# Performance work log

Hardware: AMD Instinct MI355X
Metric: run time of the kernel (lower is better)

Reference implementation:

```python
import jax, jax.numpy as jnp
import numpy as np

P = 3; Q = 3                 # spline degrees (deg_p, deg_q)
OUT_U = 64; OUT_V = 64       # surface evaluation grid
W_CTRL = 1.0; W_SURF = 1.0
B = 1024; MU_MAX = 32; MV_MAX = 32
EPS = 1e-5                   # SurfEval samples u,v in [eps, 1-eps]


def _open_uniform_knots(n_valid, degree, n_max):
    """Clamped open-uniform knot vector for n_valid ctrl pts, padded to static
    length n_max+degree+1. Entries beyond the valid span are clamped to 1.0,
    which makes the padded basis functions identically zero on [eps, 1-eps]."""
    L = n_valid + degree + 1  # true (ragged) knot count, traced int
    k = jnp.arange(n_max + degree + 1)
    interior = k.astype(jnp.float32) / (L - 1).astype(jnp.float32)
    return jnp.where(k <= degree, 0.0, jnp.where(k >= L - 1 - degree, 1.0, interior))


def _bspline_basis(kv, degree, u):
    """Cox-de Boor, vectorized over u. kv: (n_max+degree+1,), u: (U,).
    Returns (U, n_max) basis matrix; padded columns are exactly zero."""
    N = ((u[None, :] >= kv[:-1, None]) & (u[None, :] < kv[1:, None])).astype(jnp.float32)
    for d in range(1, degree + 1):
        m = N.shape[0] - 1  # number of basis funcs at this level
        den1 = kv[d:d + m] - kv[:m]
        den2 = kv[d + 1:d + 1 + m] - kv[1:1 + m]
        s1 = jnp.where((den1 > 0)[:, None],
                       (u[None, :] - kv[:m, None]) / jnp.where(den1 > 0, den1, 1.0)[:, None], 0.0)
        s2 = jnp.where((den2 > 0)[:, None],
                       (kv[d + 1:d + 1 + m, None] - u[None, :]) / jnp.where(den2 > 0, den2, 1.0)[:, None], 0.0)
        N = s1 * N[:m] + s2 * N[1:m + 1]
    return N.T  # (U, n_max)


def _eval_surface(ctrl, mask_b, u, v):
    """NURBS surface eval for one sample with ragged (Mu_i, Mv_i) via padded
    knots/basis; unit weights => rational division by basis partition sum."""
    mu = jnp.maximum(jnp.sum(jnp.any(mask_b > 0, axis=1)), P + 1)
    mv = jnp.maximum(jnp.sum(jnp.any(mask_b > 0, axis=0)), Q + 1)
    Bu = _bspline_basis(_open_uniform_knots(mu, P, MU_MAX), P, u)  # (OUT_U, MU_MAX)
    Bv = _bspline_basis(_open_uniform_knots(mv, Q, MV_MAX), Q, v)  # (OUT_V, MV_MAX)
    num = jnp.einsum('ui,vj,ijd->uvd', Bu, Bv, ctrl)               # (OUT_U, OUT_V, 3)
    den = Bu.sum(-1)[:, None] * Bv.sum(-1)[None, :]                # unit-weight denom
    return num / den[..., None]


def setup_inputs() -> dict:
    key = jax.random.key(0)
    k1, k2, k3, k4, k5 = jax.random.split(key, 5)
    # ragged true control sizes per sample, >= degree+1
    mu = jax.random.randint(k1, (B,), P + 1, MU_MAX + 1)
    mv = jax.random.randint(k2, (B,), Q + 1, MV_MAX + 1)
    mask = ((jnp.arange(MU_MAX)[None, :, None] < mu[:, None, None]) &
            (jnp.arange(MV_MAX)[None, None, :] < mv[:, None, None])).astype(jnp.float32)
    ctrl_pred_pad = jax.random.normal(k3, (B, MU_MAX, MV_MAX, 3), jnp.float32)
    ctrl_gt_pad = jax.random.normal(k4, (B, MU_MAX, MV_MAX, 3), jnp.float32)
    xyz_samples = jax.random.normal(k5, (B, OUT_U, OUT_V, 3), jnp.float32)
    return {"ctrl_pred_pad": ctrl_pred_pad, "ctrl_gt_pad": ctrl_gt_pad,
            "mask": mask, "xyz_samples": xyz_samples}


def reference(ctrl_pred_pad, ctrl_gt_pad, mask, xyz_samples):
    # masked control-point MSE
    diff2 = ((ctrl_pred_pad - ctrl_gt_pad) ** 2).sum(-1)
    loss_ctrl = (diff2 * mask).sum() / jnp.maximum(mask.sum() * 3.0, 1.0)
    # batched ragged surface evaluation
    u = jnp.linspace(EPS, 1.0 - EPS, OUT_U)
    v = jnp.linspace(EPS, 1.0 - EPS, OUT_V)
    surf = jax.vmap(lambda c, m: _eval_surface(c, m, u, v))(ctrl_pred_pad, mask)
    loss_surf = jnp.mean((surf.reshape(B, -1, 3) - xyz_samples.reshape(B, -1, 3)) ** 2)
    total = W_CTRL * loss_ctrl + W_SURF * loss_surf  # original computes total BEFORE nan-guard
    bad = jnp.isnan(surf).any() | jnp.isinf(surf).any()
    surf_mse = jnp.where(bad, jnp.float32(1e6), loss_surf)
    return total, loss_ctrl, surf_mse
```

## Files before the change

### kernel.cpp

```cpp
#include <hip/hip_runtime.h>
#include <math.h>

#define MU_MAXC 32
#define MV_MAXC 32
#define OUT_UC  64
#define OUT_VC  64
#define DEG     3
#define NKNOT   (MU_MAXC + DEG + 1)
#define EPSV    1e-5f

__global__ void zero_ws_kernel(double* acc, int* bad) {
    acc[0] = 0.0; acc[1] = 0.0; acc[2] = 0.0; bad[0] = 0;
}

__device__ __forceinline__ float kv_at(int k, int L) {
    return (k <= DEG) ? 0.f : ((k >= L - 1 - DEG) ? 1.f : (float)k / (float)(L - 1));
}

template <int MODE>
__launch_bounds__(256)
__global__ void nurbs_loss_kernel(const float* __restrict__ ctrl_pred,
                                  const float* __restrict__ ctrl_gt,
                                  const float* __restrict__ mask,
                                  const float* __restrict__ xyz,
                                  double* __restrict__ pd, int G,
                                  int* __restrict__ badp)
{
    const int bb  = blockIdx.x;
    const int s   = bb >> 1;
    const int h   = bb & 1;
    const int tid = threadIdx.x;

    __shared__ float s_tmp[32 * MV_MAXC * 3];
    __shared__ float s_Bu4[4 * 32];
    __shared__ float s_Bv4[4 * OUT_VC];
    __shared__ int   s_uoff[32];
    __shared__ int   s_voff[OUT_VC];
    __shared__ float s_invSumBu[32];
    __shared__ int   s_rowany[MU_MAXC];
    __shared__ int   s_colany[MV_MAXC];
    __shared__ int   s_mu, s_mv, s_bad;
    __shared__ float s_wred[4], s_wred2[4];
    __shared__ float s_ctrl_diff, s_ctrl_mask;

    if (tid < 32) { s_rowany[tid] = 0; s_colany[tid] = 0; }
    if (tid == 0) s_bad = 0;
    __syncthreads();

    float lsum_mask, lsum_diff = 0.f;
    float4 mm;
    {
        mm = ((const float4*)(mask + (size_t)s * 1024))[tid];
        lsum_mask = mm.x + mm.y + mm.z + mm.w;
        const int row = tid >> 3;
        const int colb = (tid & 7) * 4;
        if (lsum_mask > 0.f) s_rowany[row] = 1;
        if (mm.x > 0.f) s_colany[colb + 0] = 1;
        if (mm.y > 0.f) s_colany[colb + 1] = 1;
        if (mm.z > 0.f) s_colany[colb + 2] = 1;
        if (mm.w > 0.f) s_colany[colb + 3] = 1;
    }
    if ((tid >> 7) == h) {
        const float4* p4 = (const float4*)(ctrl_pred + (size_t)s * 3072);
        const float4* g4 = (const float4*)(ctrl_gt   + (size_t)s * 3072);
        const float4 pa = p4[3 * tid + 0], pb = p4[3 * tid + 1], pc = p4[3 * tid + 2];
        const float4 ga = g4[3 * tid + 0], gb = g4[3 * tid + 1], gc = g4[3 * tid + 2];
        const float a0 = pa.x - ga.x, a1 = pa.y - ga.y, a2 = pa.z - ga.z;
        const float b0 = pa.w - ga.w, b1 = pb.x - gb.x, b2 = pb.y - gb.y;
        const float c0 = pb.z - gb.z, c1 = pb.w - gb.w, c2 = pc.x - gc.x;
        const float e0 = pc.y - gc.y, e1 = pc.z - gc.z, e2 = pc.w - gc.w;
        lsum_diff = mm.x * (a0 * a0 + a1 * a1 + a2 * a2)
                  + mm.y * (b0 * b0 + b1 * b1 + b2 * b2)
                  + mm.z * (c0 * c0 + c1 * c1 + c2 * c2)
                  + mm.w * (e0 * e0 + e1 * e1 + e2 * e2);
    }
    lsum_mask *= 0.5f;
    #pragma unroll
    for (int off = 32; off > 0; off >>= 1) {
        lsum_mask += __shfl_down(lsum_mask, off);
        lsum_diff += __shfl_down(lsum_diff, off);
    }
    if ((tid & 63) == 0) { s_wred[tid >> 6] = lsum_mask; s_wred2[tid >> 6] = lsum_diff; }
    __syncthreads();

    if (tid == 0) {
        int cu = 0, cv = 0;
        #pragma unroll
        for (int i = 0; i < 32; i++) { cu += s_rowany[i]; cv += s_colany[i]; }
        s_mu = cu > (DEG + 1) ? cu : (DEG + 1);
        s_mv = cv > (DEG + 1) ? cv : (DEG + 1);
        s_ctrl_mask = s_wred[0] + s_wred[1] + s_wred[2] + s_wred[3];
        s_ctrl_diff = s_wred2[0] + s_wred2[1] + s_wred2[2] + s_wred2[3];
    }
    __syncthreads();

    if (tid < 96) {
        const bool isV = tid < 64;
        const int t = isV ? tid : (tid - 64);
        const int gidx = isV ? t : (32 * h + t);
        const int L = (isV ? s_mv : s_mu) + DEG + 1;
        const float step = (1.f - 2.f * EPSV) / 63.f;
        const float uu = (gidx == 63) ? (1.f - EPSV) : (EPSV + step * (float)gidx);

        int span = DEG;
        #pragma unroll
        for (int k = DEG + 1; k < NKNOT - 1; k++)
            if (kv_at(k, L) <= uu) span = k;

        float left[DEG + 1], right[DEG + 1];
        #pragma unroll
        for (int j = 1; j <= DEG; j++) {
            left[j]  = uu - kv_at(span + 1 - j, L);
            right[j] = kv_at(span + j, L) - uu;
        }
        float N4[DEG + 1];
        N4[0] = 1.f;
        #pragma unroll
        for (int j = 1; j <= DEG; j++) {
            float saved = 0.f;
            #pragma unroll
            for (int r = 0; r < j; r++) {
                const float temp = N4[r] / (right[r + 1] + left[j - r]);
                N4[r] = saved + right[r + 1] * temp;
                saved = left[j - r] * temp;
            }
            N4[j] = saved;
        }
        const float sum = N4[0] + N4[1] + N4[2] + N4[3];
        const float invs = 1.0f / sum;
        const int off = span - DEG;
        if (isV) {
            #pragma unroll
            for (int r = 0; r < 4; r++) s_Bv4[r * 64 + t] = N4[r] * invs;
            s_voff[t] = off;
        } else {
            #pragma unroll
            for (int r = 0; r < 4; r++) s_Bu4[r * 32 + t] = N4[r];
            s_uoff[t] = off; s_invSumBu[t] = invs;
        }
    }
    __syncthreads();

    {
        const float4* ctrl4 = (const float4*)(ctrl_pred + (size_t)s * 3072);
        float4* tmp4 = (float4*)s_tmp;
        #pragma unroll
        for (int k = 0; k < 3; k++) {
            const int flat4 = tid + 256 * k;
            const int lu = flat4 / 24;
            const int q = flat4 - lu * 24;
            const int off = s_uoff[lu];
            const float w0 = s_Bu4[0 * 32 + lu];
            const float w1 = s_Bu4[1 * 32 + lu];
            const float w2 = s_Bu4[2 * 32 + lu];
            const float w3 = s_Bu4[3 * 32 + lu];
            const float4 c0 = ctrl4[(off + 0) * 24 + q];
            const float4 c1 = ctrl4[(off + 1) * 24 + q];
            const float4 c2 = ctrl4[(off + 2) * 24 + q];
            const float4 c3 = ctrl4[(off + 3) * 24 + q];
            float4 a;
            a.x = w0 * c0.x + w1 * c1.x + w2 * c2.x + w3 * c3.x;
            a.y = w0 * c0.y + w1 * c1.y + w2 * c2.y + w3 * c3.y;
            a.z = w0 * c0.z + w1 * c1.z + w2 * c2.z + w3 * c3.z;
            a.w = w0 * c0.w + w1 * c1.w + w2 * c2.w + w3 * c3.w;
            tmp4[flat4] = a;
        }
    }
    __syncthreads();

    float lsum_surf = 0.f;
    int bad = 0;
    {
        const int vg   = (tid & 15) * 4;
        const int lug0 = tid >> 4;
        float w[4][4]; int vo[4];
        #pragma unroll
        for (int c = 0; c < 4; c++) {
            vo[c] = s_voff[vg + c] * 3;
            #pragma unroll
            for (int r = 0; r < 4; r++) w[c][r] = s_Bv4[r * 64 + vg + c];
        }
        #pragma unroll
        for (int k = 0; k < 2; k++) {
            const int lu = lug0 + 16 * k;
            const int u  = 32 * h + lu;
            const float inv = s_invSumBu[lu];
            const float* tp = &s_tmp[lu * 96];
            const float4* x4 = (const float4*)(xyz + ((size_t)s * 4096 + u * 64 + vg) * 3);
            const float4 xa = x4[0], xb = x4[1], xc = x4[2];
            float px[4], py[4], pz[4];
            px[0] = xa.x; py[0] = xa.y; pz[0] = xa.z;
            px[1] = xa.w; py[1] = xb.x; pz[1] = xb.y;
            px[2] = xb.z; py[2] = xb.w; pz[2] = xc.x;
            px[3] = xc.y; py[3] = xc.z; pz[3] = xc.w;
            #pragma unroll
            for (int c = 0; c < 4; c++) {
                const float* tpc = tp + vo[c];
                const float n0 = w[c][0] * tpc[0] + w[c][1] * tpc[3] + w[c][2] * tpc[6] + w[c][3] * tpc[9];
                const float n1 = w[c][0] * tpc[1] + w[c][1] * tpc[4] + w[c][2] * tpc[7] + w[c][3] * tpc[10];
                const float n2 = w[c][0] * tpc[2] + w[c][1] * tpc[5] + w[c][2] * tpc[8] + w[c][3] * tpc[11];
                const float x0 = n0 * inv, x1 = n1 * inv, x2 = n2 * inv;
                const float d0 = x0 - px[c];
                const float d1 = x1 - py[c];
                const float d2 = x2 - pz[c];
                lsum_surf += d0 * d0 + d1 * d1 + d2 * d2;
                if (!isfinite(x0) || !isfinite(x1) || !isfinite(x2)) bad = 1;
            }
        }
    }
    #pragma unroll
    for (int off = 32; off > 0; off >>= 1)
        lsum_surf += __shfl_down(lsum_surf, off);
    if ((tid & 63) == 0) s_wred[tid >> 6] = lsum_surf;
    if (bad) atomicOr(&s_bad, 1);
    __syncthreads();

    if (tid == 0) {
        const double surf = (double)s_wred[0] + s_wred[1] + s_wred[2] + s_wred[3];
        if (MODE == 0) {
            pd[bb]          = (double)s_ctrl_diff;
            pd[G + bb]      = (double)s_ctrl_mask;
            pd[2 * G + bb]  = surf;
            badp[bb]        = s_bad;
        } else {
            atomicAdd(&pd[0], (double)s_ctrl_diff);
            atomicAdd(&pd[1], (double)s_ctrl_mask);
            atomicAdd(&pd[2], surf);
            if (s_bad) atomicOr(badp, 1);
        }
    }
}

__global__ void finalize_partials_kernel(const double* __restrict__ pd,
                                         const int* __restrict__ badp,
                                         float* __restrict__ out, int G, int Bcnt)
{
    __shared__ double sd0[4], sd1[4], sd2[4];
    __shared__ int sb[4];
    const int tid = threadIdx.x;
    double a0 = 0.0, a1 = 0.0, a2 = 0.0; int bad = 0;
    for (int i = tid; i < G; i += 256) {
        a0 += pd[i]; a1 += pd[G + i]; a2 += pd[2 * G + i];
        bad |= badp[i];
    }
    #pragma unroll
    for (int off = 32; off > 0; off >>= 1) {
        a0 += __shfl_down(a0, off);
        a1 += __shfl_down(a1, off);
        a2 += __shfl_down(a2, off);
        bad |= __shfl_down(bad, off);
    }
    if ((tid & 63) == 0) { const int w = tid >> 6; sd0[w] = a0; sd1[w] = a1; sd2[w] = a2; sb[w] = bad; }
    __syncthreads();
    if (tid == 0) {
        double d0 = 0, d1 = 0, d2 = 0; int bb = 0;
        #pragma unroll
        for (int i = 0; i < 4; i++) { d0 += sd0[i]; d1 += sd1[i]; d2 += sd2[i]; bb |= sb[i]; }
        const double denc = d1 * 3.0;
        const double lc = d0 / (denc > 1.0 ? denc : 1.0);
        const double ls = d2 / ((double)Bcnt * OUT_UC * OUT_VC * 3.0);
        out[0] = (float)(lc + ls);
        out[1] = (float)lc;
        out[2] = bb ? 1.0e6f : (float)ls;
    }
}

__global__ void finalize_atomic_kernel(const double* __restrict__ acc,
                                       const int* __restrict__ bad,
                                       float* __restrict__ out, int Bcnt)
{
    const double denc = acc[1] * 3.0;
    const double lc = acc[0] / (denc > 1.0 ? denc : 1.0);
    const double ls = acc[2] / ((double)Bcnt * OUT_UC * OUT_VC * 3.0);
    out[0] = (float)(lc + ls);
    out[1] = (float)lc;
    out[2] = bad[0] ? 1.0e6f : (float)ls;
}

extern "C" void kernel_launch(void* const* d_in, const int* in_sizes, int n_in,
                              void* d_out, int out_size, void* d_ws, size_t ws_size,
                              hipStream_t stream)
{
    const float* pred = (const float*)d_in[0];
    const float* gt   = (const float*)d_in[1];
    const float* mask = (const float*)d_in[2];
    const float* xyz  = (const float*)d_in[3];
    const int Bcnt = in_sizes[2] / (MU_MAXC * MV_MAXC);
    const int G = 2 * Bcnt;

    double* pd = (double*)d_ws;
    float* out = (float*)d_out;

    const size_t need = (size_t)3 * G * sizeof(double) + (size_t)G * sizeof(int);
    if (ws_size >= need) {
        int* badp = (int*)(pd + 3 * G);
        hipLaunchKernelGGL((nurbs_loss_kernel<0>), dim3(G), dim3(256), 0, stream,
                           pred, gt, mask, xyz, pd, G, badp);
        hipLaunchKernelGGL(finalize_partials_kernel, dim3(1), dim3(256), 0, stream,
                           pd, badp, out, G, Bcnt);
    } else {
        int* badp = (int*)(pd + 3);
        hipLaunchKernelGGL(zero_ws_kernel, dim3(1), dim3(1), 0, stream, pd, badp);
        hipLaunchKernelGGL((nurbs_loss_kernel<1>), dim3(G), dim3(256), 0, stream,
                           pred, gt, mask, xyz, pd, G, badp);
        hipLaunchKernelGGL(finalize_atomic_kernel, dim3(1), dim3(1), 0, stream,
                           pd, badp, out, Bcnt);
    }
}
```

Before: 115.2 us.

## Prefetch xyz samples into LDS via async global_load_lds at kernel start

The kernel now issues the xyz sample tile for its half-surface at the very beginning as direct global-to-LDS loads. It also hoists the ctrl_pred/ctrl_gt loads ahead of the first barrier, so the memory latency overlaps the mask reduction and basis computation instead of being exposed in the final loss loop. This costs an extra 24KB of LDS per block, which may reduce occupancy. Correctness relies on the async LDS writes being complete at the first __syncthreads.

```diff
diff --git a/kernel.cpp b/kernel.cpp
--- a/kernel.cpp
+++ b/kernel.cpp
@@ -31,7 +31,8 @@
     const int h   = bb & 1;
     const int tid = threadIdx.x;
 
-    __shared__ float s_tmp[32 * MV_MAXC * 3];
+    __shared__ __align__(16) float s_xyz[32 * OUT_VC * 3];
+    __shared__ __align__(16) float s_tmp[32 * MV_MAXC * 3];
     __shared__ float s_Bu4[4 * 32];
     __shared__ float s_Bv4[4 * OUT_VC];
     __shared__ int   s_uoff[32];
@@ -45,13 +46,33 @@
 
     if (tid < 32) { s_rowany[tid] = 0; s_colany[tid] = 0; }
     if (tid == 0) s_bad = 0;
-    __syncthreads();
-
-    float lsum_mask, lsum_diff = 0.f;
-    float4 mm;
+
+    const float4 mm = ((const float4*)(mask + (size_t)s * 1024))[tid];
+    float4 pa, pb, pc, ga, gb, gc;
+    const int mine = ((tid >> 7) == h);
+    if (mine) {
+        const float4* p4 = (const float4*)(ctrl_pred + (size_t)s * 3072);
+        const float4* g4 = (const float4*)(ctrl_gt   + (size_t)s * 3072);
+        pa = p4[3 * tid + 0]; pb = p4[3 * tid + 1]; pc = p4[3 * tid + 2];
+        ga = g4[3 * tid + 0]; gb = g4[3 * tid + 1]; gc = g4[3 * tid + 2];
+    }
+
     {
-        mm = ((const float4*)(mask + (size_t)s * 1024))[tid];
-        lsum_mask = mm.x + mm.y + mm.z + mm.w;
+        const float* xsrc = xyz + ((size_t)s * 4096 + (size_t)h * 2048) * 3;
+        #pragma unroll
+        for (int w = 0; w < 6; w++) {
+            const int f4 = tid + 256 * w;
+            __builtin_amdgcn_global_load_lds(
+                (const __attribute__((address_space(1))) unsigned int*)(xsrc + f4 * 4),
+                (__attribute__((address_space(3))) unsigned int*)(s_xyz + f4 * 4),
+                16, 0, 0);
+        }
+    }
+    __syncthreads();
+
+    float lsum_mask = mm.x + mm.y + mm.z + mm.w;
+    float lsum_diff = 0.f;
+    {
         const int row = tid >> 3;
         const int colb = (tid & 7) * 4;
         if (lsum_mask > 0.f) s_rowany[row] = 1;
@@ -60,11 +81,7 @@
         if (mm.z > 0.f) s_colany[colb + 2] = 1;
         if (mm.w > 0.f) s_colany[colb + 3] = 1;
     }
-    if ((tid >> 7) == h) {
-        const float4* p4 = (const float4*)(ctrl_pred + (size_t)s * 3072);
-        const float4* g4 = (const float4*)(ctrl_gt   + (size_t)s * 3072);
-        const float4 pa = p4[3 * tid + 0], pb = p4[3 * tid + 1], pc = p4[3 * tid + 2];
-        const float4 ga = g4[3 * tid + 0], gb = g4[3 * tid + 1], gc = g4[3 * tid + 2];
+    if (mine) {
         const float a0 = pa.x - ga.x, a1 = pa.y - ga.y, a2 = pa.z - ga.z;
         const float b0 = pa.w - ga.w, b1 = pb.x - gb.x, b2 = pb.y - gb.y;
         const float c0 = pb.z - gb.z, c1 = pb.w - gb.w, c2 = pc.x - gc.x;
@@ -183,10 +200,9 @@
         #pragma unroll
         for (int k = 0; k < 2; k++) {
             const int lu = lug0 + 16 * k;
-            const int u  = 32 * h + lu;
             const float inv = s_invSumBu[lu];
             const float* tp = &s_tmp[lu * 96];
-            const float4* x4 = (const float4*)(xyz + ((size_t)s * 4096 + u * 64 + vg) * 3);
+            const float4* x4 = (const float4*)(s_xyz + (lu * 64 + vg) * 3);
             const float4 xa = x4[0], xb = x4[1], xc = x4[2];
             float px[4], py[4], pz[4];
             px[0] = xa.x; py[0] = xa.y; pz[0] = xa.z;
```

Result: slower. 119.9 us (+4.0%).
